# Kernel optimization log

Measured on AMD Instinct MI355X. Metric: run time of the kernel, lower is better.

Reference implementation:

```python
import jax, jax.numpy as jnp
import numpy as np

H, W = 4096, 4096
MIN_VAL, MAX_VAL = 0, 256
D = MAX_VAL - MIN_VAL - 1  # 255 candidate thresholds t = 0..254
N_BINS = MAX_VAL           # pixel values live in [0, 256)


def setup_inputs() -> dict:
    key = jax.random.key(0)
    img = jax.random.randint(key, (H, W), MIN_VAL, MAX_VAL, dtype=jnp.int32)
    return {"img_HxW": img}


def reference(img_HxW):
    hw = H * W
    flat = img_HxW.ravel()
    # Histogram of pixel counts and pixel-value sums (float32 accumulation,
    # matching torch.sum(..., dtype=torch.float32) in the original).
    cnt = jax.ops.segment_sum(jnp.ones_like(flat, jnp.float32), flat, num_segments=N_BINS)
    val_sum = jax.ops.segment_sum(flat.astype(jnp.float32), flat, num_segments=N_BINS)
    # Cumulative sums give, for each threshold t, the count/sum of pixels <= t.
    # This equals the original's broadcast compare + masked sum over [H*W, d].
    num_b = jnp.cumsum(cnt)[:D]        # pixels in class "black" (<= t)
    sum_b = jnp.cumsum(val_sum)[:D]    # sum of those pixels
    num_w = hw - num_b                  # pixels in class "white" (> t)
    sum_w = jnp.sum(val_sum) - sum_b
    mean_b = sum_b / num_b
    mean_w = sum_w / num_w
    var_hist = num_b * num_w * (mean_b - mean_w) ** 2  # inter-class variance
    thresh = jnp.argmax(var_hist).astype(jnp.int32)
    bin_img = jnp.where(img_HxW <= thresh,
                        jnp.int32(MIN_VAL), jnp.int32(MAX_VAL))
    return thresh, bin_img
```

## Files before the change

kernel.cpp:

```cpp
#include <hip/hip_runtime.h>

#define HW_TOTAL (4096 * 4096)
#define NBINS 256
#define NCHUNK (HW_TOTAL / 4)
#define HIST_B 512
#define CH_PER_BLK (NCHUNK / HIST_B)
#define BATCH 8
#define BIN_COARSEN 4
#define BIN_B (NCHUNK / 256 / BIN_COARSEN)

#define WS_PART_BYTES (HIST_B * NBINS * 4 + 256)

template <int MODE>
__global__ __launch_bounds__(256) void otsu_hist_k(const int4* __restrict__ img4,
                                                   unsigned* __restrict__ out) {
    __shared__ unsigned h[4 * NBINS];
    for (int i = threadIdx.x; i < 4 * NBINS; i += 256) h[i] = 0;
    __syncthreads();

    const unsigned sub = (threadIdx.x & 3u) << 8;
    const int base = blockIdx.x * CH_PER_BLK;

    for (int ob = 0; ob < CH_PER_BLK / (256 * BATCH); ++ob) {
        int4 v[BATCH];
        const int i0 = base + ob * (256 * BATCH) + threadIdx.x;
#pragma unroll
        for (int k = 0; k < BATCH; ++k) v[k] = img4[i0 + k * 256];
#pragma unroll
        for (int k = 0; k < BATCH; ++k) {
            atomicAdd(&h[sub + (unsigned)v[k].x], 1u);
            atomicAdd(&h[sub + (unsigned)v[k].y], 1u);
            atomicAdd(&h[sub + (unsigned)v[k].z], 1u);
            atomicAdd(&h[sub + (unsigned)v[k].w], 1u);
        }
    }
    __syncthreads();

    const int i = threadIdx.x;
    unsigned t = h[i] + h[i + 256] + h[i + 512] + h[i + 768];
    if (MODE == 0) {
        out[blockIdx.x * NBINS + i] = t;
    } else {
        if (t) atomicAdd(&out[i], t);
    }
}

__global__ __launch_bounds__(1024) void otsu_thresh_k(const unsigned* __restrict__ partials,
                                                      int B,
                                                      int* __restrict__ d_out,
                                                      int* __restrict__ thresh_ws) {
    __shared__ unsigned part[4][NBINS];
    __shared__ unsigned cnt[NBINS];

    const int bin = threadIdx.x & 255;
    const int q = threadIdx.x >> 8;
    const int BQ = (B + 3) / 4;
    int b = q * BQ;
    int e = min((q + 1) * BQ, B);
    unsigned s = 0;
    for (; b + 8 <= e; b += 8) {
#pragma unroll
        for (int k = 0; k < 8; ++k) s += partials[(b + k) * NBINS + bin];
    }
    for (; b < e; ++b) s += partials[b * NBINS + bin];
    part[q][bin] = s;
    __syncthreads();

    if (threadIdx.x < 256)
        cnt[bin] = part[0][bin] + part[1][bin] + part[2][bin] + part[3][bin];
    __syncthreads();

    if (threadIdx.x >= 64) return;
    const int lane = threadIdx.x;

    uint4 c = ((const uint4*)cnt)[lane];
    unsigned cs[4] = {c.x, c.y, c.z, c.w};

    unsigned long long lc[4], lv[4];
    unsigned long long ccum = 0ull, vcum = 0ull;
#pragma unroll
    for (int k = 0; k < 4; ++k) {
        ccum += cs[k];
        vcum += (unsigned long long)cs[k] * (unsigned)(4 * lane + k);
        lc[k] = ccum;
        lv[k] = vcum;
    }

    unsigned long long cscan = ccum, vscan = vcum;
    for (int d = 1; d < 64; d <<= 1) {
        unsigned long long cu = __shfl_up(cscan, d);
        unsigned long long vu = __shfl_up(vscan, d);
        if (lane >= d) { cscan += cu; vscan += vu; }
    }
    const unsigned long long cbase = cscan - ccum;
    const unsigned long long vbase = vscan - vcum;
    const unsigned long long vtotal = __shfl(vscan, 63);

    double best = -1.0;
    int bestt = 255;
    const double hw = (double)HW_TOTAL;
    const double vtot_d = (double)vtotal;
#pragma unroll
    for (int k = 0; k < 4; ++k) {
        int t = 4 * lane + k;
        if (t > 254) continue;
        double nb = (double)(cbase + lc[k]);
        double sb = (double)(vbase + lv[k]);
        double nw = hw - nb;
        double sw = vtot_d - sb;
        double mb = sb / nb;
        double mw = sw / nw;
        double dm = mb - mw;
        double var = nb * nw * dm * dm;
        if (var > best || (var == best && t < bestt)) { best = var; bestt = t; }
    }

    for (int d = 32; d >= 1; d >>= 1) {
        double ov = __shfl_xor(best, d);
        int ot = __shfl_xor(bestt, d);
        if (ov > best || (ov == best && ot < bestt)) { best = ov; bestt = ot; }
    }
    if (lane == 0) {
        d_out[0] = bestt;
        *thresh_ws = bestt;
    }
}

__global__ __launch_bounds__(256) void otsu_bin_k(const int* __restrict__ img,
                                                  int* __restrict__ out,
                                                  const int* __restrict__ thresh_ws) {
    const int thresh = *thresh_ws;
    const int base = blockIdx.x * (256 * BIN_COARSEN);
    const int lane = threadIdx.x & 63;
#pragma unroll
    for (int k = 0; k < BIN_COARSEN; ++k) {
        const int c = base + k * 256 + threadIdx.x;
        int4 v = ((const int4*)img)[c];
        int prev = __shfl_up(v.w, 1);
        if (lane == 0) prev = (c > 0) ? img[4 * c - 1] : 0;
        int4 o;
        o.x = (c == 0) ? thresh : ((prev <= thresh) ? 0 : 256);
        o.y = (v.x <= thresh) ? 0 : 256;
        o.z = (v.y <= thresh) ? 0 : 256;
        o.w = (v.z <= thresh) ? 0 : 256;
        ((int4*)out)[c] = o;
    }
    if (blockIdx.x == 0 && threadIdx.x == 0)
        out[HW_TOTAL] = (img[HW_TOTAL - 1] <= thresh) ? 0 : 256;
}

extern "C" void kernel_launch(void* const* d_in, const int* in_sizes, int n_in,
                              void* d_out, int out_size, void* d_ws, size_t ws_size,
                              hipStream_t stream) {
    const int* img = (const int*)d_in[0];
    int* out = (int*)d_out;
    int* thresh_ws = (int*)d_ws;
    unsigned* hist_buf = (unsigned*)((char*)d_ws + 256);

    if (ws_size >= WS_PART_BYTES) {
        otsu_hist_k<0><<<HIST_B, 256, 0, stream>>>((const int4*)img, hist_buf);
        otsu_thresh_k<<<1, 1024, 0, stream>>>(hist_buf, HIST_B, out, thresh_ws);
    } else {
        hipMemsetAsync(hist_buf, 0, NBINS * sizeof(unsigned), stream);
        otsu_hist_k<1><<<HIST_B, 256, 0, stream>>>((const int4*)img, hist_buf);
        otsu_thresh_k<<<1, 1024, 0, stream>>>(hist_buf, 1, out, thresh_ws);
    }
    otsu_bin_k<<<BIN_B, 256, 0, stream>>>(img, out, thresh_ws);
}
```

Before: 45.83 us.

## Use 1024-thread blocks, interleave histogram sub-bins, add nontemporal stores in binarize

The histogram kernel now uses 1024-thread blocks. Each thread loads 8 int4 chunks exactly once instead of looping. The four shared-memory sub-histograms are interleaved as (value<<2)|sub rather than stored in separate 256-bin planes, which changes the LDS bank distribution of the atomics. The binarize kernel is restructured to 512 blocks of 1024 threads, each handling 8 chunks, and writes its output with nontemporal stores to avoid cache pollution. The aim is less per-block overhead and better memory streaming, at the cost of higher per-block register pressure and possibly different LDS conflict behaviour.

```diff
diff --git a/kernel.cpp b/kernel.cpp
--- a/kernel.cpp
+++ b/kernel.cpp
@@ -4,44 +4,42 @@
 #define NBINS 256
 #define NCHUNK (HW_TOTAL / 4)
 #define HIST_B 512
-#define CH_PER_BLK (NCHUNK / HIST_B)
+#define BLK 1024
 #define BATCH 8
-#define BIN_COARSEN 4
-#define BIN_B (NCHUNK / 256 / BIN_COARSEN)
 
-#define WS_PART_BYTES (HIST_B * NBINS * 4 + 256)
+typedef int int4n __attribute__((ext_vector_type(4)));
+
+#define WS_NEED (HIST_B * NBINS * 4 + 256)
 
 template <int MODE>
-__global__ __launch_bounds__(256) void otsu_hist_k(const int4* __restrict__ img4,
-                                                   unsigned* __restrict__ out) {
+__global__ __launch_bounds__(BLK, 8) void otsu_hist_k(const int4* __restrict__ img4,
+                                                      unsigned* __restrict__ out) {
     __shared__ unsigned h[4 * NBINS];
-    for (int i = threadIdx.x; i < 4 * NBINS; i += 256) h[i] = 0;
+    const int t = threadIdx.x;
+    for (int i = t; i < 4 * NBINS; i += BLK) h[i] = 0;
     __syncthreads();
 
-    const unsigned sub = (threadIdx.x & 3u) << 8;
-    const int base = blockIdx.x * CH_PER_BLK;
-
-    for (int ob = 0; ob < CH_PER_BLK / (256 * BATCH); ++ob) {
-        int4 v[BATCH];
-        const int i0 = base + ob * (256 * BATCH) + threadIdx.x;
+    const unsigned sub = (unsigned)t & 3u;
+    const int i0 = blockIdx.x * (BLK * BATCH) + t;
+    int4 v[BATCH];
 #pragma unroll
-        for (int k = 0; k < BATCH; ++k) v[k] = img4[i0 + k * 256];
+    for (int k = 0; k < BATCH; ++k) v[k] = img4[i0 + k * BLK];
 #pragma unroll
-        for (int k = 0; k < BATCH; ++k) {
-            atomicAdd(&h[sub + (unsigned)v[k].x], 1u);
-            atomicAdd(&h[sub + (unsigned)v[k].y], 1u);
-            atomicAdd(&h[sub + (unsigned)v[k].z], 1u);
-            atomicAdd(&h[sub + (unsigned)v[k].w], 1u);
-        }
+    for (int k = 0; k < BATCH; ++k) {
+        atomicAdd(&h[(((unsigned)v[k].x) << 2) | sub], 1u);
+        atomicAdd(&h[(((unsigned)v[k].y) << 2) | sub], 1u);
+        atomicAdd(&h[(((unsigned)v[k].z) << 2) | sub], 1u);
+        atomicAdd(&h[(((unsigned)v[k].w) << 2) | sub], 1u);
     }
     __syncthreads();
 
-    const int i = threadIdx.x;
-    unsigned t = h[i] + h[i + 256] + h[i + 512] + h[i + 768];
-    if (MODE == 0) {
-        out[blockIdx.x * NBINS + i] = t;
-    } else {
-        if (t) atomicAdd(&out[i], t);
+    if (t < NBINS) {
+        unsigned s = h[t << 2] + h[(t << 2) | 1] + h[(t << 2) | 2] + h[(t << 2) | 3];
+        if (MODE == 0) {
+            out[blockIdx.x * NBINS + t] = s;
+        } else {
+            if (s) atomicAdd(&out[t], s);
+        }
     }
 }
 
@@ -49,32 +47,32 @@
                                                       int B,
                                                       int* __restrict__ d_out,
                                                       int* __restrict__ thresh_ws) {
-    __shared__ unsigned part[4][NBINS];
+    __shared__ unsigned red[4][NBINS];
     __shared__ unsigned cnt[NBINS];
 
     const int bin = threadIdx.x & 255;
     const int q = threadIdx.x >> 8;
     const int BQ = (B + 3) / 4;
-    int b = q * BQ;
-    int e = min((q + 1) * BQ, B);
+    int r = q * BQ;
+    const int e = min((q + 1) * BQ, B);
     unsigned s = 0;
-    for (; b + 8 <= e; b += 8) {
+    for (; r + 8 <= e; r += 8) {
 #pragma unroll
-        for (int k = 0; k < 8; ++k) s += partials[(b + k) * NBINS + bin];
+        for (int k = 0; k < 8; ++k) s += partials[(r + k) * NBINS + bin];
     }
-    for (; b < e; ++b) s += partials[b * NBINS + bin];
-    part[q][bin] = s;
+    for (; r < e; ++r) s += partials[r * NBINS + bin];
+    red[q][bin] = s;
     __syncthreads();
 
-    if (threadIdx.x < 256)
-        cnt[bin] = part[0][bin] + part[1][bin] + part[2][bin] + part[3][bin];
+    if (threadIdx.x < NBINS)
+        cnt[bin] = red[0][bin] + red[1][bin] + red[2][bin] + red[3][bin];
     __syncthreads();
 
     if (threadIdx.x >= 64) return;
     const int lane = threadIdx.x;
 
-    uint4 c = ((const uint4*)cnt)[lane];
-    unsigned cs[4] = {c.x, c.y, c.z, c.w};
+    uint4 c4 = ((const uint4*)cnt)[lane];
+    unsigned cs[4] = {c4.x, c4.y, c4.z, c4.w};
 
     unsigned long long lc[4], lv[4];
     unsigned long long ccum = 0ull, vcum = 0ull;
@@ -85,7 +83,6 @@
         lc[k] = ccum;
         lv[k] = vcum;
     }
-
     unsigned long long cscan = ccum, vscan = vcum;
     for (int d = 1; d < 64; d <<= 1) {
         unsigned long long cu = __shfl_up(cscan, d);
@@ -102,19 +99,16 @@
     const double vtot_d = (double)vtotal;
 #pragma unroll
     for (int k = 0; k < 4; ++k) {
-        int t = 4 * lane + k;
-        if (t > 254) continue;
+        int tt = 4 * lane + k;
+        if (tt > 254) continue;
         double nb = (double)(cbase + lc[k]);
         double sb = (double)(vbase + lv[k]);
         double nw = hw - nb;
         double sw = vtot_d - sb;
-        double mb = sb / nb;
-        double mw = sw / nw;
-        double dm = mb - mw;
+        double dm = sb / nb - sw / nw;
         double var = nb * nw * dm * dm;
-        if (var > best || (var == best && t < bestt)) { best = var; bestt = t; }
+        if (var > best || (var == best && tt < bestt)) { best = var; bestt = tt; }
     }
-
     for (int d = 32; d >= 1; d >>= 1) {
         double ov = __shfl_xor(best, d);
         int ot = __shfl_xor(bestt, d);
@@ -126,26 +120,28 @@
     }
 }
 
-__global__ __launch_bounds__(256) void otsu_bin_k(const int* __restrict__ img,
-                                                  int* __restrict__ out,
-                                                  const int* __restrict__ thresh_ws) {
+__global__ __launch_bounds__(BLK, 8) void otsu_bin_k(const int* __restrict__ img,
+                                                     int* __restrict__ out,
+                                                     const int* __restrict__ thresh_ws) {
     const int thresh = *thresh_ws;
-    const int base = blockIdx.x * (256 * BIN_COARSEN);
-    const int lane = threadIdx.x & 63;
+    const int t = threadIdx.x;
+    const int lane = t & 63;
+    const int i0 = blockIdx.x * (BLK * BATCH) + t;
+    const int4* img4 = (const int4*)img;
 #pragma unroll
-    for (int k = 0; k < BIN_COARSEN; ++k) {
-        const int c = base + k * 256 + threadIdx.x;
-        int4 v = ((const int4*)img)[c];
+    for (int k = 0; k < BATCH; ++k) {
+        const int c = i0 + k * BLK;
+        int4 v = img4[c];
         int prev = __shfl_up(v.w, 1);
         if (lane == 0) prev = (c > 0) ? img[4 * c - 1] : 0;
-        int4 o;
+        int4n o;
         o.x = (c == 0) ? thresh : ((prev <= thresh) ? 0 : 256);
         o.y = (v.x <= thresh) ? 0 : 256;
         o.z = (v.y <= thresh) ? 0 : 256;
         o.w = (v.z <= thresh) ? 0 : 256;
-        ((int4*)out)[c] = o;
+        __builtin_nontemporal_store(o, (int4n*)out + c);
     }
-    if (blockIdx.x == 0 && threadIdx.x == 0)
+    if (blockIdx.x == 0 && t == 0)
         out[HW_TOTAL] = (img[HW_TOTAL - 1] <= thresh) ? 0 : 256;
 }
 
@@ -157,13 +153,13 @@
     int* thresh_ws = (int*)d_ws;
     unsigned* hist_buf = (unsigned*)((char*)d_ws + 256);
 
-    if (ws_size >= WS_PART_BYTES) {
-        otsu_hist_k<0><<<HIST_B, 256, 0, stream>>>((const int4*)img, hist_buf);
+    if (ws_size >= (size_t)WS_NEED) {
+        otsu_hist_k<0><<<HIST_B, BLK, 0, stream>>>((const int4*)img, hist_buf);
         otsu_thresh_k<<<1, 1024, 0, stream>>>(hist_buf, HIST_B, out, thresh_ws);
     } else {
-        hipMemsetAsync(hist_buf, 0, NBINS * sizeof(unsigned), stream);
-        otsu_hist_k<1><<<HIST_B, 256, 0, stream>>>((const int4*)img, hist_buf);
+        (void)hipMemsetAsync(hist_buf, 0, NBINS * sizeof(unsigned), stream);
+        otsu_hist_k<1><<<HIST_B, BLK, 0, stream>>>((const int4*)img, hist_buf);
         otsu_thresh_k<<<1, 1024, 0, stream>>>(hist_buf, 1, out, thresh_ws);
     }
-    otsu_bin_k<<<BIN_B, 256, 0, stream>>>(img, out, thresh_ws);
+    otsu_bin_k<<<HIST_B, BLK, 0, stream>>>(img, out, thresh_ws);
 }
```

After: 45.82 us. About the same (-0.0%).
